# Optimization experiments

Hardware: AMD Instinct MI355X
Metric: run time of the kernel (lower is better)

Reference implementation:

```python
import jax, jax.numpy as jnp
import numpy as np

POS_DIM = 3
CAPACITY = 262144  # 2**18 hash-table slots per level
NR_LEVELS = 24
NR_FEAT = 2
N_POINTS = 524288
HASH_MUL = 2531011  # permutohedral-lattice hash multiplier (uint32 wraparound)


def _permuto_encode(positions, lattice_values, random_shift, anneal_window, scale_per_level):
    # positions: [N,d]  lattice_values: [L,C,F]  random_shift: [L,d]
    # anneal_window: [L]  scale_per_level: [L]
    N, d = positions.shape
    L, C, F = lattice_values.shape
    dp1 = d + 1
    dim = jnp.arange(d, dtype=positions.dtype)
    # per-level, per-axis scale: s_l / sqrt((i+1)(i+2))
    scale_factor = scale_per_level[:, None] / jnp.sqrt((dim + 1.0) * (dim + 2.0))  # [L,d]
    cf = (positions[None, :, :] + random_shift[:, None, :]) * scale_factor[:, None, :]  # [L,N,d]
    # elevate onto the hyperplane sum(x)=0 in R^{d+1}:
    # elevated[0]=sum(cf); elevated[i]=sum(cf[i:]) - i*cf[i-1]
    S = jnp.cumsum(cf[..., ::-1], axis=-1)[..., ::-1]            # suffix sums S[i]=sum cf[i:]
    S_next = jnp.concatenate([S[..., 1:], jnp.zeros_like(S[..., :1])], axis=-1)
    i_arr = jnp.arange(1, dp1, dtype=positions.dtype)
    elevated = jnp.concatenate([S[..., :1], S_next - i_arr * cf], axis=-1)  # [L,N,d+1]
    # nearest remainder-0 lattice point (round each coord to multiple of d+1)
    v = elevated / dp1
    up = jnp.ceil(v) * dp1
    down = jnp.floor(v) * dp1
    rem0 = jnp.where(up - elevated < elevated - down, up, down)  # [L,N,d+1]
    sum_val = jnp.round(jnp.sum(rem0, axis=-1) / dp1).astype(jnp.int32)  # [L,N]
    # rank: for i<j, if diff_i < diff_j then rank_i++ else rank_j++
    diff = elevated - rem0
    di = diff[..., :, None]
    dj = diff[..., None, :]
    ii = jnp.arange(dp1)[:, None]
    jj = jnp.arange(dp1)[None, :]
    rank = jnp.sum(jnp.where(jj > ii, dj > di, (jj < ii) & (dj >= di)), axis=-1).astype(jnp.int32)
    rank = rank + sum_val[..., None]
    under = rank < 0
    over = rank > d
    rank = rank + dp1 * under.astype(jnp.int32) - dp1 * over.astype(jnp.int32)
    rem0 = rem0 + dp1 * (under.astype(rem0.dtype) - over.astype(rem0.dtype))
    # barycentric weights: bary[d-rank_i] += delta_i; bary[d+1-rank_i] -= delta_i; bary[0] += 1 + bary[d+1]
    delta = (elevated - rem0) / dp1  # [L,N,d+1]
    t = d - rank
    bary = []
    for k in range(dp1 + 1):
        mk = (t == k).astype(delta.dtype) - (t == k - 1).astype(delta.dtype)
        bary.append(jnp.sum(delta * mk, axis=-1))  # [L,N]
    bary[0] = bary[0] + 1.0 + bary[dp1]
    # hash the d+1 simplex vertices; key[i] = rem0[i] + r - (d+1)*[rank[i] > d-r]
    rem0i = jnp.round(rem0).astype(jnp.int32)
    r = jnp.arange(dp1, dtype=jnp.int32)  # remainder axis -> simplex vertex
    h = jnp.zeros((L, N, dp1), dtype=jnp.uint32)
    for i in range(d):  # tiny structural loop over pos_dim
        key_i = rem0i[..., i:i + 1] + r - dp1 * (rank[..., i:i + 1] > d - r).astype(jnp.int32)
        h = (h + key_i.astype(jnp.uint32)) * jnp.uint32(HASH_MUL)
    ix = (h % jnp.uint32(C)).astype(jnp.int32)  # [L,N,d+1]
    # gather the d+1 vertex feature vectors per level and blend barycentrically
    gather = jax.vmap(lambda table, idx: table[idx])  # vmap over levels
    out = jnp.zeros((L, N, F), dtype=lattice_values.dtype)
    for rr in range(dp1):  # tiny structural loop over simplex vertices
        out = out + bary[rr][..., None] * gather(lattice_values, ix[..., rr])
    out = out * anneal_window[:, None, None]
    # kernel outputs [L,F,N] -> permute(2,0,1).reshape(N, L*F)
    return jnp.transpose(out, (1, 0, 2)).reshape(N, L * F)


def setup_inputs() -> dict:
    key = jax.random.key(0)
    k1, k2, k3 = jax.random.split(key, 3)
    positions = jax.random.uniform(k1, (N_POINTS, POS_DIM), dtype=jnp.float32)
    lattice_values = jax.random.normal(k2, (NR_LEVELS, CAPACITY, NR_FEAT), dtype=jnp.float32) * 1e-5
    random_shift = jax.random.normal(k3, (NR_LEVELS, POS_DIM), dtype=jnp.float32) * 10.0
    anneal_window = jnp.ones((NR_LEVELS,), dtype=jnp.float32)
    scale_per_level = jnp.asarray(np.geomspace(16.0, 2048.0, NR_LEVELS), dtype=jnp.float32)
    return {"positions": positions, "lattice_values": lattice_values,
            "random_shift": random_shift, "anneal_window": anneal_window,
            "scale_per_level": scale_per_level}


def reference(positions, lattice_values, random_shift, anneal_window, scale_per_level):
    return _permuto_encode(positions, lattice_values, random_shift, anneal_window, scale_per_level)
```

## Files before the change

### kernel.cpp

```cpp
#include <hip/hip_runtime.h>
#include <cstdint>

#define NPOINTS 524288
#define NLEV 24
#define CAP 262144
#define HASHMUL 2531011u
#define PTS_PER_BLOCK 512
#define BLOCKS_PER_LEVEL (NPOINTS / PTS_PER_BLOCK)

#define NBUCKET 32768
#define WS_H_B   ((size_t)NLEV * NPOINTS * 4)
#define POS4_B   ((size_t)NPOINTS * 16)
#define HIST_B   ((size_t)NBUCKET * 4)

typedef float v2f  __attribute__((ext_vector_type(2)));
typedef float v4f  __attribute__((ext_vector_type(4)));
typedef _Float16 f16x2 __attribute__((ext_vector_type(2)));


__device__ __forceinline__ uint32_t expand_bits(uint32_t v) {
    v = (v | (v << 16)) & 0x030000FFu;
    v = (v | (v << 8))  & 0x0300F00Fu;
    v = (v | (v << 4))  & 0x030C30C3u;
    v = (v | (v << 2))  & 0x09249249u;
    return v;
}

__device__ __forceinline__ uint32_t morton5(float x, float y, float z) {
    int xi = (int)(x * 32.0f); xi = xi < 0 ? 0 : (xi > 31 ? 31 : xi);
    int yi = (int)(y * 32.0f); yi = yi < 0 ? 0 : (yi > 31 ? 31 : yi);
    int zi = (int)(z * 32.0f); zi = zi < 0 ? 0 : (zi > 31 ? 31 : zi);
    return expand_bits((uint32_t)xi) | (expand_bits((uint32_t)yi) << 1)
         | (expand_bits((uint32_t)zi) << 2);
}

__global__ __launch_bounds__(256) void hist_kernel(
    const float* __restrict__ pos, int* __restrict__ hist) {
    int n = blockIdx.x * 256 + threadIdx.x;
    float x = pos[n*3+0], y = pos[n*3+1], z = pos[n*3+2];
    atomicAdd(&hist[morton5(x, y, z)], 1);
}

__global__ __launch_bounds__(256) void scan_kernel(
    const int* __restrict__ hist, int* __restrict__ offs) {
    __shared__ int sums[256];
    const int t = threadIdx.x;
    const int CHUNK = NBUCKET / 256;
    const int4* h4 = reinterpret_cast<const int4*>(hist) + t * (CHUNK/4);
    int s = 0;
    #pragma unroll
    for (int i = 0; i < CHUNK/4; ++i) { int4 v = h4[i]; s += v.x + v.y + v.z + v.w; }
    sums[t] = s;
    __syncthreads();
    for (int d = 1; d < 256; d <<= 1) {
        int v = (t >= d) ? sums[t - d] : 0;
        __syncthreads();
        sums[t] += v;
        __syncthreads();
    }
    int run = sums[t] - s;
    int4* o4 = reinterpret_cast<int4*>(offs) + t * (CHUNK/4);
    #pragma unroll
    for (int i = 0; i < CHUNK/4; ++i) {
        int4 v = h4[i]; int4 o;
        o.x = run; run += v.x;
        o.y = run; run += v.y;
        o.z = run; run += v.z;
        o.w = run; run += v.w;
        o4[i] = o;
    }
}

__global__ __launch_bounds__(256) void scatter_kernel(
    const float* __restrict__ pos, int* __restrict__ offs,
    v4f* __restrict__ pos4) {
    int n = blockIdx.x * 256 + threadIdx.x;
    float x = pos[n*3+0], y = pos[n*3+1], z = pos[n*3+2];
    uint32_t code = morton5(x, y, z);
    int slot = atomicAdd(&offs[code], 1);
    v4f v; v.x = x; v.y = y; v.z = z; v.w = __uint_as_float((uint32_t)n);
    pos4[slot] = v;
}


__device__ __forceinline__ void prep_point(
    const float p0, const float p1, const float p2,
    const float sf0, const float sf1, const float sf2,
    const float sh0, const float sh1, const float sh2,
    uint32_t* __restrict__ ix, float* __restrict__ w)
{
    const float cf0 = (p0 + sh0) * sf0;
    const float cf1 = (p1 + sh1) * sf1;
    const float cf2 = (p2 + sh2) * sf2;

    const float S2 = cf2;
    const float S1 = cf2 + cf1;
    const float S0 = S1 + cf0;

    float E[4];
    E[0] = S0;
    E[1] = S1 - 1.0f*cf0;
    E[2] = S2 - 2.0f*cf1;
    E[3] = 0.0f - 3.0f*cf2;

    float rem0[4];
    float sumrem = 0.0f;
    #pragma unroll
    for (int i = 0; i < 4; ++i) {
        float v  = E[i] * 0.25f;
        float up = ceilf(v)  * 4.0f;
        float dn = floorf(v) * 4.0f;
        rem0[i] = (up - E[i] < E[i] - dn) ? up : dn;
        sumrem += rem0[i];
    }
    const int sum_val = (int)rintf(sumrem * 0.25f);

    float diff[4];
    #pragma unroll
    for (int i = 0; i < 4; ++i) diff[i] = E[i] - rem0[i];

    int rank[4];
    #pragma unroll
    for (int i = 0; i < 4; ++i) {
        int rk = 0;
        #pragma unroll
        for (int j = 0; j < 4; ++j) {
            if (j > i)      rk += (diff[j] >  diff[i]) ? 1 : 0;
            else if (j < i) rk += (diff[j] >= diff[i]) ? 1 : 0;
        }
        rk += sum_val;
        if (rk < 0)      { rk += 4; rem0[i] += 4.0f; }
        else if (rk > 3) { rk -= 4; rem0[i] -= 4.0f; }
        rank[i] = rk;
    }

    float delta[4];
    #pragma unroll
    for (int i = 0; i < 4; ++i) delta[i] = (E[i] - rem0[i]) * 0.25f;

    float b[5];
    #pragma unroll
    for (int k = 0; k < 5; ++k) {
        float acc = 0.0f;
        #pragma unroll
        for (int i = 0; i < 4; ++i) {
            int ti = 3 - rank[i];
            float m = ((ti == k) ? 1.0f : 0.0f) - ((ti == (k-1)) ? 1.0f : 0.0f);
            acc += delta[i] * m;
        }
        b[k] = acc;
    }
    b[0] += 1.0f + b[4];

    int rem0i[4];
    #pragma unroll
    for (int i = 0; i < 4; ++i) rem0i[i] = (int)rintf(rem0[i]);

    #pragma unroll
    for (int r = 0; r < 4; ++r) {
        uint32_t h = 0u;
        #pragma unroll
        for (int i = 0; i < 3; ++i) {
            int key = rem0i[i] + r - 4 * ((rank[i] > 3 - r) ? 1 : 0);
            h = (h + (uint32_t)key) * HASHMUL;
        }
        ix[r] = h & (uint32_t)(CAP - 1);
        w[r]  = b[r];
    }
}

__device__ __forceinline__ uint32_t pack_h2_scaled(float x, float y) {
    f16x2 ph;
    ph.x = (_Float16)(x * 256.0f);
    ph.y = (_Float16)(y * 256.0f);
    return __builtin_bit_cast(uint32_t, ph);
}

__global__ __launch_bounds__(256, 6) void permuto_kernel(
    const v4f* __restrict__ pos4,
    const float* __restrict__ lattice,
    const float* __restrict__ shift,
    const float* __restrict__ anneal,
    const float* __restrict__ scale,
    uint32_t* __restrict__ ws_u)
{
    __shared__ v4f s_pos[PTS_PER_BLOCK];

    const int t    = threadIdx.x;
    const int bid  = blockIdx.x;
    const int xcd  = bid & 7;
    const int slot = bid >> 3;
    const int l    = xcd + 8 * (slot >> 10);
    const int nb   = slot & (BLOCKS_PER_LEVEL - 1);
    const int pbase = nb * PTS_PER_BLOCK;

    {
        const v4f* src = pos4 + pbase;
        s_pos[t]       = src[t];
        s_pos[t + 256] = src[t + 256];
    }

    const float sc  = scale[l];
    const float sf0 = sc / sqrtf(2.0f);
    const float sf1 = sc / sqrtf(6.0f);
    const float sf2 = sc / sqrtf(12.0f);
    const float sh0 = shift[l*3+0];
    const float sh1 = shift[l*3+1];
    const float sh2 = shift[l*3+2];
    const float an  = anneal[l];

    __syncthreads();

    const v4f pA = s_pos[t];
    const v4f pB = s_pos[t + 256];

    uint32_t ixA[4], ixB[4];
    float    wA[4],  wB[4];
    prep_point(pA.x, pA.y, pA.z, sf0, sf1, sf2, sh0, sh1, sh2, ixA, wA);
    prep_point(pB.x, pB.y, pB.z, sf0, sf1, sf2, sh0, sh1, sh2, ixB, wB);

    const v2f* __restrict__ tbl =
        reinterpret_cast<const v2f*>(lattice) + (size_t)l * CAP;

    v2f vA[4], vB[4];
    #pragma unroll
    for (int r = 0; r < 4; ++r) vA[r] = tbl[ixA[r]];
    #pragma unroll
    for (int r = 0; r < 4; ++r) vB[r] = tbl[ixB[r]];

    float oA0 = 0.f, oA1 = 0.f, oB0 = 0.f, oB1 = 0.f;
    #pragma unroll
    for (int r = 0; r < 4; ++r) {
        oA0 += wA[r] * vA[r].x;  oA1 += wA[r] * vA[r].y;
        oB0 += wB[r] * vB[r].x;  oB1 += wB[r] * vB[r].y;
    }

    const uint32_t uA = pack_h2_scaled(oA0 * an, oA1 * an);
    const uint32_t uB = pack_h2_scaled(oB0 * an, oB1 * an);

    uint32_t* pWA = ws_u + (size_t)l * NPOINTS + pbase + t;
    __builtin_nontemporal_store(uA, pWA);
    __builtin_nontemporal_store(uB, pWA + 256);
}

__global__ __launch_bounds__(256) void transpose_kernel(
    const uint32_t* __restrict__ ws_u,
    const uint32_t* __restrict__ pos4u,
    float* __restrict__ out)
{
    const int t  = threadIdx.x;
    const int m  = t & 3;
    const int p  = blockIdx.x * 64 + (t >> 2);

    const uint32_t orig = pos4u[4*p + 3];

    float r[12];
    #pragma unroll
    for (int i = 0; i < 6; ++i) {
        const int l = m * 6 + i;
        const uint32_t u = ws_u[(size_t)l * NPOINTS + p];
        const f16x2 hh = __builtin_bit_cast(f16x2, u);
        r[2*i+0] = (float)hh.x * 0.00390625f;
        r[2*i+1] = (float)hh.y * 0.00390625f;
    }

    float* orow = out + (size_t)orig * 48 + m * 12;
    #pragma unroll
    for (int j = 0; j < 3; ++j) {
        v4f v; v.x = r[4*j]; v.y = r[4*j+1]; v.z = r[4*j+2]; v.w = r[4*j+3];
        *reinterpret_cast<v4f*>(orow + 4*j) = v;
    }
}

__global__ __launch_bounds__(256) void permuto_direct(
    const float* __restrict__ pos,
    const float* __restrict__ lattice,
    const float* __restrict__ shift,
    const float* __restrict__ anneal,
    const float* __restrict__ scale,
    float* __restrict__ out)
{
    const int tid = blockIdx.x * 256 + threadIdx.x;
    const int n = tid / NLEV;
    const int l = tid - n * NLEV;

    const float sc  = scale[l];
    const float sf0 = sc / sqrtf(2.0f);
    const float sf1 = sc / sqrtf(6.0f);
    const float sf2 = sc / sqrtf(12.0f);

    uint32_t ix[4]; float w[4];
    prep_point(pos[n*3+0], pos[n*3+1], pos[n*3+2],
               sf0, sf1, sf2, shift[l*3+0], shift[l*3+1], shift[l*3+2], ix, w);

    const v2f* tbl = reinterpret_cast<const v2f*>(lattice) + (size_t)l * CAP;
    float o0 = 0.f, o1 = 0.f;
    #pragma unroll
    for (int r = 0; r < 4; ++r) {
        v2f v = tbl[ix[r]];
        o0 += w[r] * v.x;  o1 += w[r] * v.y;
    }
    const float an = anneal[l];
    v2f res; res.x = o0 * an; res.y = o1 * an;
    *reinterpret_cast<v2f*>(out + (size_t)n * (NLEV*2) + l*2) = res;
}

extern "C" void kernel_launch(void* const* d_in, const int* in_sizes, int n_in,
                              void* d_out, int out_size, void* d_ws, size_t ws_size,
                              hipStream_t stream) {
    const float* pos     = (const float*)d_in[0];
    const float* lattice = (const float*)d_in[1];
    const float* shift   = (const float*)d_in[2];
    const float* anneal  = (const float*)d_in[3];
    const float* scale   = (const float*)d_in[4];
    float* out = (float*)d_out;

    uint8_t* w8 = (uint8_t*)d_ws;
    uint32_t* ws_u = (uint32_t*)w8;
    v4f*      pos4 = (v4f*)(w8 + WS_H_B);
    int*      hist = (int*)(w8 + WS_H_B + POS4_B);
    int*      offs = (int*)(w8 + WS_H_B + POS4_B + HIST_B);
    const size_t need = WS_H_B + POS4_B + 2 * HIST_B;

    if (ws_size >= need) {
        hipMemsetAsync(hist, 0, HIST_B, stream);
        hist_kernel<<<NPOINTS / 256, 256, 0, stream>>>(pos, hist);
        scan_kernel<<<1, 256, 0, stream>>>(hist, offs);
        scatter_kernel<<<NPOINTS / 256, 256, 0, stream>>>(pos, offs, pos4);
        permuto_kernel<<<NLEV * BLOCKS_PER_LEVEL, 256, 0, stream>>>(
            pos4, lattice, shift, anneal, scale, ws_u);
        transpose_kernel<<<NPOINTS / 64, 256, 0, stream>>>(
            ws_u, (const uint32_t*)pos4, out);
    } else {
        permuto_direct<<<(NPOINTS * NLEV) / 256, 256, 0, stream>>>(
            pos, lattice, shift, anneal, scale, out);
    }
}
```

Measured before the change: 271.1 us.

## Replace global-atomic Morton bucketing with per-block shared-memory histograms and scans

The point-sorting pre-pass now uses 64 blocks that each build a 4096-bucket histogram in shared memory, followed by a three-stage scan (column totals, global prefix, per-block bases) and a scatter that uses shared-memory atomics instead of global atomics. This removes heavy global atomic contention and the memset. The Morton grid also shrinks from 32^3 to 16^3 cells, giving coarser spatial locality for the main kernel. The cost is only 64 blocks doing the sort, which underuses the GPU and runs long serial per-thread loops, plus three extra launches.

```diff
diff --git a/kernel.cpp b/kernel.cpp
--- a/kernel.cpp
+++ b/kernel.cpp
@@ -8,10 +8,15 @@
 #define PTS_PER_BLOCK 512
 #define BLOCKS_PER_LEVEL (NPOINTS / PTS_PER_BLOCK)
 
-#define NBUCKET 32768
+#define NBUCKET 4096
+#define SORT_BLOCKS 64
+#define SORT_PTS (NPOINTS / SORT_BLOCKS)
+
 #define WS_H_B   ((size_t)NLEV * NPOINTS * 4)
 #define POS4_B   ((size_t)NPOINTS * 16)
-#define HIST_B   ((size_t)NBUCKET * 4)
+#define PART_B   ((size_t)SORT_BLOCKS * NBUCKET * 4)
+#define BASE_B   PART_B
+#define TOT_B    ((size_t)NBUCKET * 4)
 
 typedef float v2f  __attribute__((ext_vector_type(2)));
 typedef float v4f  __attribute__((ext_vector_type(4)));
@@ -26,30 +31,49 @@
     return v;
 }
 
-__device__ __forceinline__ uint32_t morton5(float x, float y, float z) {
-    int xi = (int)(x * 32.0f); xi = xi < 0 ? 0 : (xi > 31 ? 31 : xi);
-    int yi = (int)(y * 32.0f); yi = yi < 0 ? 0 : (yi > 31 ? 31 : yi);
-    int zi = (int)(z * 32.0f); zi = zi < 0 ? 0 : (zi > 31 ? 31 : zi);
+__device__ __forceinline__ uint32_t morton4(float x, float y, float z) {
+    int xi = (int)(x * 16.0f); xi = xi < 0 ? 0 : (xi > 15 ? 15 : xi);
+    int yi = (int)(y * 16.0f); yi = yi < 0 ? 0 : (yi > 15 ? 15 : yi);
+    int zi = (int)(z * 16.0f); zi = zi < 0 ? 0 : (zi > 15 ? 15 : zi);
     return expand_bits((uint32_t)xi) | (expand_bits((uint32_t)yi) << 1)
          | (expand_bits((uint32_t)zi) << 2);
 }
 
 __global__ __launch_bounds__(256) void hist_kernel(
-    const float* __restrict__ pos, int* __restrict__ hist) {
-    int n = blockIdx.x * 256 + threadIdx.x;
-    float x = pos[n*3+0], y = pos[n*3+1], z = pos[n*3+2];
-    atomicAdd(&hist[morton5(x, y, z)], 1);
-}
-
-__global__ __launch_bounds__(256) void scan_kernel(
-    const int* __restrict__ hist, int* __restrict__ offs) {
+    const float* __restrict__ pos, int* __restrict__ part) {
+    __shared__ int h[NBUCKET];
+    const int t = threadIdx.x, b = blockIdx.x;
+    #pragma unroll
+    for (int i = t; i < NBUCKET; i += 256) h[i] = 0;
+    __syncthreads();
+    const int n0 = b * SORT_PTS;
+    for (int i = 0; i < SORT_PTS / 256; ++i) {
+        const int n = n0 + i * 256 + t;
+        atomicAdd(&h[morton4(pos[n*3], pos[n*3+1], pos[n*3+2])], 1);
+    }
+    __syncthreads();
+    #pragma unroll
+    for (int i = t; i < NBUCKET; i += 256) part[b * NBUCKET + i] = h[i];
+}
+
+__global__ __launch_bounds__(256) void scanA_kernel(
+    const int* __restrict__ part, int* __restrict__ tot) {
+    const int j = blockIdx.x * 256 + threadIdx.x;
+    int s = 0;
+    #pragma unroll 8
+    for (int b = 0; b < SORT_BLOCKS; ++b) s += part[b * NBUCKET + j];
+    tot[j] = s;
+}
+
+__global__ __launch_bounds__(256) void scanB_kernel(
+    const int* __restrict__ tot, int* __restrict__ G) {
     __shared__ int sums[256];
     const int t = threadIdx.x;
-    const int CHUNK = NBUCKET / 256;
-    const int4* h4 = reinterpret_cast<const int4*>(hist) + t * (CHUNK/4);
+    const int CH = NBUCKET / 256;
+    int loc[CH];
     int s = 0;
     #pragma unroll
-    for (int i = 0; i < CHUNK/4; ++i) { int4 v = h4[i]; s += v.x + v.y + v.z + v.w; }
+    for (int k = 0; k < CH; ++k) { loc[k] = tot[t * CH + k]; s += loc[k]; }
     sums[t] = s;
     __syncthreads();
     for (int d = 1; d < 256; d <<= 1) {
@@ -59,27 +83,38 @@
         __syncthreads();
     }
     int run = sums[t] - s;
-    int4* o4 = reinterpret_cast<int4*>(offs) + t * (CHUNK/4);
-    #pragma unroll
-    for (int i = 0; i < CHUNK/4; ++i) {
-        int4 v = h4[i]; int4 o;
-        o.x = run; run += v.x;
-        o.y = run; run += v.y;
-        o.z = run; run += v.z;
-        o.w = run; run += v.w;
-        o4[i] = o;
+    #pragma unroll
+    for (int k = 0; k < CH; ++k) { G[t * CH + k] = run; run += loc[k]; }
+}
+
+__global__ __launch_bounds__(256) void scanC_kernel(
+    const int* __restrict__ part, const int* __restrict__ G,
+    int* __restrict__ base) {
+    const int j = blockIdx.x * 256 + threadIdx.x;
+    int run = G[j];
+    #pragma unroll 8
+    for (int b = 0; b < SORT_BLOCKS; ++b) {
+        base[b * NBUCKET + j] = run;
+        run += part[b * NBUCKET + j];
     }
 }
 
 __global__ __launch_bounds__(256) void scatter_kernel(
-    const float* __restrict__ pos, int* __restrict__ offs,
+    const float* __restrict__ pos, const int* __restrict__ base,
     v4f* __restrict__ pos4) {
-    int n = blockIdx.x * 256 + threadIdx.x;
-    float x = pos[n*3+0], y = pos[n*3+1], z = pos[n*3+2];
-    uint32_t code = morton5(x, y, z);
-    int slot = atomicAdd(&offs[code], 1);
-    v4f v; v.x = x; v.y = y; v.z = z; v.w = __uint_as_float((uint32_t)n);
-    pos4[slot] = v;
+    __shared__ int cnt[NBUCKET];
+    const int t = threadIdx.x, b = blockIdx.x;
+    #pragma unroll
+    for (int i = t; i < NBUCKET; i += 256) cnt[i] = base[b * NBUCKET + i];
+    __syncthreads();
+    const int n0 = b * SORT_PTS;
+    for (int i = 0; i < SORT_PTS / 256; ++i) {
+        const int n = n0 + i * 256 + t;
+        const float x = pos[n*3], y = pos[n*3+1], z = pos[n*3+2];
+        const int slot = atomicAdd(&cnt[morton4(x, y, z)], 1);
+        v4f v; v.x = x; v.y = y; v.z = z; v.w = __uint_as_float((uint32_t)n);
+        pos4[slot] = v;
+    }
 }
 
 
@@ -316,17 +351,20 @@
     float* out = (float*)d_out;
 
     uint8_t* w8 = (uint8_t*)d_ws;
-    uint32_t* ws_u = (uint32_t*)w8;
-    v4f*      pos4 = (v4f*)(w8 + WS_H_B);
-    int*      hist = (int*)(w8 + WS_H_B + POS4_B);
-    int*      offs = (int*)(w8 + WS_H_B + POS4_B + HIST_B);
-    const size_t need = WS_H_B + POS4_B + 2 * HIST_B;
+    uint32_t* ws_u  = (uint32_t*)w8;
+    v4f*      pos4  = (v4f*)(w8 + WS_H_B);
+    int*      part  = (int*)(w8 + WS_H_B + POS4_B);
+    int*      basep = (int*)(w8 + WS_H_B + POS4_B + PART_B);
+    int*      tot   = (int*)(w8 + WS_H_B + POS4_B + PART_B + BASE_B);
+    int*      G     = (int*)(w8 + WS_H_B + POS4_B + PART_B + BASE_B + TOT_B);
+    const size_t need = WS_H_B + POS4_B + PART_B + BASE_B + 2 * TOT_B;
 
     if (ws_size >= need) {
-        hipMemsetAsync(hist, 0, HIST_B, stream);
-        hist_kernel<<<NPOINTS / 256, 256, 0, stream>>>(pos, hist);
-        scan_kernel<<<1, 256, 0, stream>>>(hist, offs);
-        scatter_kernel<<<NPOINTS / 256, 256, 0, stream>>>(pos, offs, pos4);
+        hist_kernel   <<<SORT_BLOCKS, 256, 0, stream>>>(pos, part);
+        scanA_kernel  <<<NBUCKET / 256, 256, 0, stream>>>(part, tot);
+        scanB_kernel  <<<1, 256, 0, stream>>>(tot, G);
+        scanC_kernel  <<<NBUCKET / 256, 256, 0, stream>>>(part, G, basep);
+        scatter_kernel<<<SORT_BLOCKS, 256, 0, stream>>>(pos, basep, pos4);
         permuto_kernel<<<NLEV * BLOCKS_PER_LEVEL, 256, 0, stream>>>(
             pos4, lattice, shift, anneal, scale, ws_u);
         transpose_kernel<<<NPOINTS / 64, 256, 0, stream>>>(
```

After: 239.0 us. 11.9% less time.
